# Optimization experiments

Hardware: AMD Instinct MI355X
Metric: run time of the kernel (lower is better)

## Reference

```python
import jax, jax.numpy as jnp
import numpy as np

EMBED_DIM = 1024
NUM_HEADS = 16
HEAD_DIM = EMBED_DIM // NUM_HEADS
BATCH = 2
SEQ = 2048


def setup_inputs() -> dict:
    key = jax.random.key(0)
    ks = jax.random.split(key, 9)
    s = EMBED_DIM ** -0.5
    inp = {"x": jax.random.normal(ks[0], (BATCH, SEQ, EMBED_DIM), dtype=jnp.float32)}
    names = ["Wq", "Wk", "Wv", "Wo"]
    for i, n in enumerate(names):
        inp[n] = jax.random.normal(ks[1 + i], (EMBED_DIM, EMBED_DIM), dtype=jnp.float32) * s
        inp["b" + n[1]] = jax.random.normal(ks[5 + i], (EMBED_DIM,), dtype=jnp.float32) * 0.02
    return inp


def reference(x, Wq, bq, Wk, bk, Wv, bv, Wo, bo):
    B, S, E = x.shape
    H, D = NUM_HEADS, HEAD_DIM
    scaling = D ** -0.5
    # projections (torch Linear: x @ W.T + b), reshape to (B, H, S, D)
    q = (x @ Wq.T + bq).reshape(B, S, H, D).transpose(0, 2, 1, 3)
    k = (x @ Wk.T + bk).reshape(B, S, H, D).transpose(0, 2, 1, 3)
    v = (x @ Wv.T + bv).reshape(B, S, H, D).transpose(0, 2, 1, 3)
    # full materialized score matrix, matching the original module
    scores = jnp.einsum("bhqd,bhkd->bhqk", q, k) * scaling
    causal = jnp.triu(jnp.ones((S, S), dtype=bool), k=1)  # True above diagonal
    scores = jnp.where(causal[None, None], -jnp.inf, scores)
    attn = jax.nn.softmax(scores, axis=-1)
    out = jnp.einsum("bhqk,bhkd->bhqd", attn, v)  # (B, H, S, D)
    out = out.transpose(0, 2, 1, 3).reshape(B, S, E)
    return out @ Wo.T + bo
```

## Files before the change

### kernel.cpp

```cpp
#include <hip/hip_runtime.h>
#include <stdint.h>

typedef __bf16 bf16;
typedef __bf16 bf16x8 __attribute__((ext_vector_type(8)));
typedef __bf16 bf16x4 __attribute__((ext_vector_type(4)));
typedef float  f32x4  __attribute__((ext_vector_type(4)));

#define E_DIM 1024
#define S_LEN 2048
#define BATCH 2
#define NH 16
#define DH 64

#define NEG_INF (-__builtin_inff())

__device__ __forceinline__ void load_lds16(const bf16* g, bf16* l) {
    __builtin_amdgcn_global_load_lds(
        (const __attribute__((address_space(1))) void*)g,
        (__attribute__((address_space(3))) void*)l, 16, 0, 0);
}

__global__ __launch_bounds__(256) void convert_kernel(
    const float* __restrict__ s0, const float* __restrict__ s1,
    const float* __restrict__ s2, const float* __restrict__ s3,
    const float* __restrict__ s4,
    bf16* __restrict__ d0, bf16* __restrict__ d1, bf16* __restrict__ d2,
    bf16* __restrict__ d3, bf16* __restrict__ d4,
    int n0, int n1)
{
    const float* src; bf16* dst; int n;
    switch (blockIdx.y) {
        case 0:  src = s0; dst = d0; n = n0; break;
        case 1:  src = s1; dst = d1; n = n1; break;
        case 2:  src = s2; dst = d2; n = n1; break;
        case 3:  src = s3; dst = d3; n = n1; break;
        default: src = s4; dst = d4; n = n1; break;
    }
    int i = (blockIdx.x * 256 + threadIdx.x) * 4;
    if (i >= n) return;
    float4 v = *(const float4*)(src + i);
    bf16x4 o;
    o[0] = (bf16)v.x; o[1] = (bf16)v.y; o[2] = (bf16)v.z; o[3] = (bf16)v.w;
    *(bf16x4*)(dst + i) = o;
}

__global__ __launch_bounds__(256) void gemm_kernel(
    const bf16* __restrict__ A,
    const bf16* __restrict__ W0, const bf16* __restrict__ W1, const bf16* __restrict__ W2,
    const float* __restrict__ bias0, const float* __restrict__ bias1, const float* __restrict__ bias2,
    bf16* __restrict__ outQ, bf16* __restrict__ outK, bf16* __restrict__ outVt,
    float* __restrict__ outF, int final_mode)
{
    __shared__ bf16 As[2][128 * 32];
    __shared__ bf16 Bs[2][128 * 32];

    int mode;
    const bf16* W; const float* bias;
    if (final_mode) { mode = 3; W = W0; bias = bias0; }
    else {
        mode = blockIdx.z;
        W    = (mode == 0) ? W0 : (mode == 1 ? W1 : W2);
        bias = (mode == 0) ? bias0 : (mode == 1 ? bias1 : bias2);
    }

    const int bm = blockIdx.y * 128, bn = blockIdx.x * 128;
    const int t = threadIdx.x;
    const int lane = t & 63, w = t >> 6;
    const int quad = lane >> 4, l16 = lane & 15;
    const int wm = (w & 1) * 64, wn = (w >> 1) * 64;

    const int r0 = w * 16;
    const int srow = r0 + (lane >> 2), scol = (lane & 3) * 8;
    const bf16* Ag0 = A + (size_t)(bm + srow) * E_DIM + scol;
    const bf16* Ag1 = Ag0 + (size_t)64 * E_DIM;
    const bf16* Wg0 = W + (size_t)(bn + srow) * E_DIM + scol;
    const bf16* Wg1 = Wg0 + (size_t)64 * E_DIM;

    f32x4 acc[4][4];
#pragma unroll
    for (int i = 0; i < 4; i++)
#pragma unroll
        for (int j = 0; j < 4; j++) acc[i][j] = f32x4{0.f, 0.f, 0.f, 0.f};

    load_lds16(Ag0, As[0] + r0 * 32);
    load_lds16(Ag1, As[0] + (64 + r0) * 32);
    load_lds16(Wg0, Bs[0] + r0 * 32);
    load_lds16(Wg1, Bs[0] + (64 + r0) * 32);

    int cur = 0;
    for (int kt = 0; kt < E_DIM; kt += 32) {
        __syncthreads();

        if (kt + 32 < E_DIM) {
            const int nxt = cur ^ 1;
            load_lds16(Ag0 + kt + 32, As[nxt] + r0 * 32);
            load_lds16(Ag1 + kt + 32, As[nxt] + (64 + r0) * 32);
            load_lds16(Wg0 + kt + 32, Bs[nxt] + r0 * 32);
            load_lds16(Wg1 + kt + 32, Bs[nxt] + (64 + r0) * 32);
        }

        bf16x8 af[4], bfr[4];
#pragma unroll
        for (int i = 0; i < 4; i++)
            af[i] = *(const bf16x8*)(As[cur] + (wm + i * 16 + l16) * 32 + quad * 8);
#pragma unroll
        for (int j = 0; j < 4; j++)
            bfr[j] = *(const bf16x8*)(Bs[cur] + (wn + j * 16 + l16) * 32 + quad * 8);
#pragma unroll
        for (int i = 0; i < 4; i++)
#pragma unroll
            for (int j = 0; j < 4; j++)
                acc[i][j] = __builtin_amdgcn_mfma_f32_16x16x32_bf16(af[i], bfr[j], acc[i][j], 0, 0, 0);

        cur ^= 1;
    }

#pragma unroll
    for (int j = 0; j < 4; j++) {
        const int n = bn + wn + j * 16 + l16;
        const float bv = bias[n];
#pragma unroll
        for (int i = 0; i < 4; i++) {
            const int m0 = bm + wm + i * 16 + quad * 4;
            if (mode == 3) {
#pragma unroll
                for (int r = 0; r < 4; r++)
                    outF[(size_t)(m0 + r) * E_DIM + n] = acc[i][j][r] + bv;
            } else if (mode == 2) {
                const int b_ = m0 >> 11, s0 = m0 & (S_LEN - 1);
                const int h = n >> 6, d = n & 63;
                bf16x4 pv;
#pragma unroll
                for (int r = 0; r < 4; r++) pv[r] = (bf16)(acc[i][j][r] + bv);
                *(bf16x4*)(outVt + ((size_t)((b_ * NH + h) * DH + d)) * S_LEN + s0) = pv;
            } else {
                bf16* o = (mode == 0) ? outQ : outK;
                const float sc = (mode == 0) ? 0.125f : 1.0f;
                const int h = n >> 6, d = n & 63;
#pragma unroll
                for (int r = 0; r < 4; r++) {
                    const int m = m0 + r;
                    const int b_ = m >> 11, s = m & (S_LEN - 1);
                    o[((size_t)(b_ * NH + h) * S_LEN + s) * DH + d] = (bf16)((acc[i][j][r] + bv) * sc);
                }
            }
        }
    }
}

__global__ __launch_bounds__(512, 2) void attn_kernel(
    const bf16* __restrict__ Qb, const bf16* __restrict__ Kb,
    const bf16* __restrict__ Vtb, bf16* __restrict__ Ob)
{
    __shared__ bf16 Ks[128 * 72];
    __shared__ bf16 Vs[64 * 136];
    __shared__ bf16 Ps[8][16 * 136];

    const int t = threadIdx.x, lane = t & 63, w = t >> 6;
    const int quad = lane >> 4, l16 = lane & 15;

    const int i = blockIdx.x;
    const int xcd = i & 7, rr = i >> 3;
    const int bh = (xcd << 2) | (rr & 3);
    const int pr = rr >> 2;
    const int qlo = pr, qhi = 15 - pr;

    const bf16* Qg = Qb + (size_t)bh * S_LEN * DH;
    const bf16* Kg = Kb + (size_t)bh * S_LEN * DH;
    const bf16* Vg = Vtb + (size_t)bh * DH * S_LEN;
    const int b_ = bh >> 4, h = bh & 15;
    bf16* Og = Ob + (size_t)b_ * S_LEN * E_DIM + h * DH;

    bf16* Pw = Ps[w];
    const int inrow0 = w * 16;

    bf16x8 aq[2][2];
#pragma unroll
    for (int qt = 0; qt < 2; qt++) {
        const int qrow0 = (qt ? qhi : qlo) * 128 + inrow0;
        const bf16* qp = Qg + (size_t)(qrow0 + l16) * DH + quad * 8;
        aq[qt][0] = *(const bf16x8*)(qp);
        aq[qt][1] = *(const bf16x8*)(qp + 32);
    }

    f32x4 o[2][4];
    float l_part[2][4];
#pragma unroll
    for (int qt = 0; qt < 2; qt++)
#pragma unroll
        for (int dt = 0; dt < 4; dt++) {
            o[qt][dt] = f32x4{0.f, 0.f, 0.f, 0.f};
            l_part[qt][dt] = 0.f;
        }

    const int T = qhi + 1;
    const int kr0 = t >> 3, kce = (t & 7) * 8;
    const int vr0 = t >> 4, vce = (t & 15) * 8;

    for (int kt = 0; kt < T; kt++) {
        const int kb = kt * 128;
        uint4 k0 = *(const uint4*)(Kg + (size_t)(kb + kr0) * DH + kce);
        uint4 k1 = *(const uint4*)(Kg + (size_t)(kb + kr0 + 64) * DH + kce);
        uint4 v0 = *(const uint4*)(Vg + (size_t)vr0 * S_LEN + kb + vce);
        uint4 v1 = *(const uint4*)(Vg + (size_t)(vr0 + 32) * S_LEN + kb + vce);
        __syncthreads();
        *(uint4*)(Ks + kr0 * 72 + kce) = k0;
        *(uint4*)(Ks + (kr0 + 64) * 72 + kce) = k1;
        *(uint4*)(Vs + vr0 * 136 + vce) = v0;
        *(uint4*)(Vs + (vr0 + 32) * 136 + vce) = v1;
        __syncthreads();

#pragma unroll
        for (int qt = 0; qt < 2; qt++) {
            if (qt == 0 && kt > qlo) continue;
            const bool diag = qt ? (kt == qhi) : (kt == qlo);
            const int irb = inrow0 + quad * 4;

#pragma unroll
            for (int jt = 0; jt < 8; jt++) {
                const bf16* kp = Ks + (jt * 16 + l16) * 72 + quad * 8;
                bf16x8 bk0 = *(const bf16x8*)(kp);
                bf16x8 bk1 = *(const bf16x8*)(kp + 32);
                f32x4 s = f32x4{0.f, 0.f, 0.f, 0.f};
                s = __builtin_amdgcn_mfma_f32_16x16x32_bf16(aq[qt][0], bk0, s, 0, 0, 0);
                s = __builtin_amdgcn_mfma_f32_16x16x32_bf16(aq[qt][1], bk1, s, 0, 0, 0);
                const int kcol = jt * 16 + l16;
#pragma unroll
                for (int r = 0; r < 4; r++) {
                    float sval = s[r];
                    if (diag && kcol > irb + r) sval = NEG_INF;
                    const float pe = __expf(sval);
                    l_part[qt][r] += pe;
                    Pw[(quad * 4 + r) * 136 + jt * 16 + l16] = (bf16)pe;
                }
            }

#pragma unroll
            for (int ks = 0; ks < 4; ks++) {
                bf16x8 ap = *(const bf16x8*)(Pw + l16 * 136 + ks * 32 + quad * 8);
#pragma unroll
                for (int dt = 0; dt < 4; dt++) {
                    bf16x8 bv = *(const bf16x8*)(Vs + (dt * 16 + l16) * 136 + ks * 32 + quad * 8);
                    o[qt][dt] = __builtin_amdgcn_mfma_f32_16x16x32_bf16(ap, bv, o[qt][dt], 0, 0, 0);
                }
            }
        }
    }

#pragma unroll
    for (int qt = 0; qt < 2; qt++) {
        const int qrow0 = (qt ? qhi : qlo) * 128 + inrow0;
#pragma unroll
        for (int r = 0; r < 4; r++) {
            float l = l_part[qt][r];
            l += __shfl_xor(l, 1);
            l += __shfl_xor(l, 2);
            l += __shfl_xor(l, 4);
            l += __shfl_xor(l, 8);
            l_part[qt][r] = 1.0f / l;
        }
#pragma unroll
        for (int r = 0; r < 4; r++) {
            const int srow = qrow0 + quad * 4 + r;
#pragma unroll
            for (int dt = 0; dt < 4; dt++)
                Og[(size_t)srow * E_DIM + dt * 16 + l16] =
                    (bf16)(o[qt][dt][r] * l_part[qt][r]);
        }
    }
}

extern "C" void kernel_launch(void* const* d_in, const int* in_sizes, int n_in,
                              void* d_out, int out_size, void* d_ws, size_t ws_size,
                              hipStream_t stream)
{
    const float* x  = (const float*)d_in[0];
    const float* Wq = (const float*)d_in[1];
    const float* bq = (const float*)d_in[2];
    const float* Wk = (const float*)d_in[3];
    const float* bk = (const float*)d_in[4];
    const float* Wv = (const float*)d_in[5];
    const float* bv = (const float*)d_in[6];
    const float* Wo = (const float*)d_in[7];
    const float* bo = (const float*)d_in[8];
    float* out = (float*)d_out;

    char* ws = (char*)d_ws;
    const size_t MB = 1ull << 20;
    bf16* xb  = (bf16*)(ws + 0);
    bf16* wqb = (bf16*)(ws + 8 * MB);
    bf16* wkb = (bf16*)(ws + 10 * MB);
    bf16* wvb = (bf16*)(ws + 12 * MB);
    bf16* wob = (bf16*)(ws + 14 * MB);
    bf16* Qb  = (bf16*)(ws + 16 * MB);
    bf16* Kb  = (bf16*)(ws + 24 * MB);
    bf16* Vtb = (bf16*)(ws + 32 * MB);
    bf16* Ab  = (bf16*)(ws + 40 * MB);

    convert_kernel<<<dim3(4096, 5), 256, 0, stream>>>(
        x, Wq, Wk, Wv, Wo, xb, wqb, wkb, wvb, wob, 4194304, 1048576);

    gemm_kernel<<<dim3(8, 32, 3), 256, 0, stream>>>(
        xb, wqb, wkb, wvb, bq, bk, bv, Qb, Kb, Vtb, nullptr, 0);

    attn_kernel<<<dim3(256), 512, 0, stream>>>(Qb, Kb, Vtb, Ab);

    gemm_kernel<<<dim3(8, 32, 1), 256, 0, stream>>>(
        Ab, wob, wob, wob, bo, bo, bo, nullptr, nullptr, nullptr, out, 1);
}
```

Measured before the change: 197.8 us.

## Fuse fp32-to-bf16 conversion into GEMM loads and pad LDS rows

Removes the separate convert kernel and has the GEMM read fp32 x and weights directly, converting to bf16 in registers before storing into LDS. Loads move from direct global-to-LDS to register-staged prefetch, and LDS rows are padded (32->40 in GEMM, 136->140 for P in attention) to cut bank conflicts. This removes one launch and the intermediate bf16 round trip, at the cost of re-reading fp32 x and weights from each tile (twice the bytes per reload) and more register pressure.

```diff
diff --git a/kernel.cpp b/kernel.cpp
--- a/kernel.cpp
+++ b/kernel.cpp
@@ -14,48 +14,25 @@
 
 #define NEG_INF (-__builtin_inff())
 
-__device__ __forceinline__ void load_lds16(const bf16* g, bf16* l) {
-    __builtin_amdgcn_global_load_lds(
-        (const __attribute__((address_space(1))) void*)g,
-        (__attribute__((address_space(3))) void*)l, 16, 0, 0);
+__device__ __forceinline__ bf16x8 cvt8(float4 u0, float4 u1) {
+    bf16x8 v;
+    v[0] = (bf16)u0.x; v[1] = (bf16)u0.y; v[2] = (bf16)u0.z; v[3] = (bf16)u0.w;
+    v[4] = (bf16)u1.x; v[5] = (bf16)u1.y; v[6] = (bf16)u1.z; v[7] = (bf16)u1.w;
+    return v;
 }
 
-__global__ __launch_bounds__(256) void convert_kernel(
-    const float* __restrict__ s0, const float* __restrict__ s1,
-    const float* __restrict__ s2, const float* __restrict__ s3,
-    const float* __restrict__ s4,
-    bf16* __restrict__ d0, bf16* __restrict__ d1, bf16* __restrict__ d2,
-    bf16* __restrict__ d3, bf16* __restrict__ d4,
-    int n0, int n1)
-{
-    const float* src; bf16* dst; int n;
-    switch (blockIdx.y) {
-        case 0:  src = s0; dst = d0; n = n0; break;
-        case 1:  src = s1; dst = d1; n = n1; break;
-        case 2:  src = s2; dst = d2; n = n1; break;
-        case 3:  src = s3; dst = d3; n = n1; break;
-        default: src = s4; dst = d4; n = n1; break;
-    }
-    int i = (blockIdx.x * 256 + threadIdx.x) * 4;
-    if (i >= n) return;
-    float4 v = *(const float4*)(src + i);
-    bf16x4 o;
-    o[0] = (bf16)v.x; o[1] = (bf16)v.y; o[2] = (bf16)v.z; o[3] = (bf16)v.w;
-    *(bf16x4*)(dst + i) = o;
-}
-
 __global__ __launch_bounds__(256) void gemm_kernel(
-    const bf16* __restrict__ A,
-    const bf16* __restrict__ W0, const bf16* __restrict__ W1, const bf16* __restrict__ W2,
+    const float* __restrict__ Af, const bf16* __restrict__ Abf,
+    const float* __restrict__ W0, const float* __restrict__ W1, const float* __restrict__ W2,
     const float* __restrict__ bias0, const float* __restrict__ bias1, const float* __restrict__ bias2,
     bf16* __restrict__ outQ, bf16* __restrict__ outK, bf16* __restrict__ outVt,
     float* __restrict__ outF, int final_mode)
 {
-    __shared__ bf16 As[2][128 * 32];
-    __shared__ bf16 Bs[2][128 * 32];
+    __shared__ bf16 As[2][128 * 40];
+    __shared__ bf16 Bs[2][128 * 40];
 
     int mode;
-    const bf16* W; const float* bias;
+    const float* W; const float* bias;
     if (final_mode) { mode = 3; W = W0; bias = bias0; }
     else {
         mode = blockIdx.z;
@@ -69,12 +46,15 @@
     const int quad = lane >> 4, l16 = lane & 15;
     const int wm = (w & 1) * 64, wn = (w >> 1) * 64;
 
-    const int r0 = w * 16;
-    const int srow = r0 + (lane >> 2), scol = (lane & 3) * 8;
-    const bf16* Ag0 = A + (size_t)(bm + srow) * E_DIM + scol;
-    const bf16* Ag1 = Ag0 + (size_t)64 * E_DIM;
-    const bf16* Wg0 = W + (size_t)(bn + srow) * E_DIM + scol;
-    const bf16* Wg1 = Wg0 + (size_t)64 * E_DIM;
+    const int r1 = t >> 2,          o1 = (t & 3) * 8;
+    const int r2 = (t + 256) >> 2,  o2 = (t & 3) * 8;
+
+    const float* Wg1 = W + (size_t)(bn + r1) * E_DIM + o1;
+    const float* Wg2 = W + (size_t)(bn + r2) * E_DIM + o2;
+    const float* Ag1f = Af  ? Af  + (size_t)(bm + r1) * E_DIM + o1 : nullptr;
+    const float* Ag2f = Af  ? Af  + (size_t)(bm + r2) * E_DIM + o2 : nullptr;
+    const bf16*  Ag1b = Abf ? Abf + (size_t)(bm + r1) * E_DIM + o1 : nullptr;
+    const bf16*  Ag2b = Abf ? Abf + (size_t)(bm + r2) * E_DIM + o2 : nullptr;
 
     f32x4 acc[4][4];
 #pragma unroll
@@ -82,30 +62,53 @@
 #pragma unroll
         for (int j = 0; j < 4; j++) acc[i][j] = f32x4{0.f, 0.f, 0.f, 0.f};
 
-    load_lds16(Ag0, As[0] + r0 * 32);
-    load_lds16(Ag1, As[0] + (64 + r0) * 32);
-    load_lds16(Wg0, Bs[0] + r0 * 32);
-    load_lds16(Wg1, Bs[0] + (64 + r0) * 32);
+    float4 wa0, wa1, wb0, wb1;
+    float4 aa0, aa1, ab0, ab1;
+    bf16x8 ba1, ba2;
+
+    wa0 = *(const float4*)(Wg1);  wa1 = *(const float4*)(Wg1 + 4);
+    wb0 = *(const float4*)(Wg2);  wb1 = *(const float4*)(Wg2 + 4);
+    if (final_mode) {
+        ba1 = *(const bf16x8*)(Ag1b);
+        ba2 = *(const bf16x8*)(Ag2b);
+    } else {
+        aa0 = *(const float4*)(Ag1f); aa1 = *(const float4*)(Ag1f + 4);
+        ab0 = *(const float4*)(Ag2f); ab1 = *(const float4*)(Ag2f + 4);
+    }
 
     int cur = 0;
     for (int kt = 0; kt < E_DIM; kt += 32) {
+        if (final_mode) {
+            *(bf16x8*)(As[cur] + r1 * 40 + o1) = ba1;
+            *(bf16x8*)(As[cur] + r2 * 40 + o2) = ba2;
+        } else {
+            *(bf16x8*)(As[cur] + r1 * 40 + o1) = cvt8(aa0, aa1);
+            *(bf16x8*)(As[cur] + r2 * 40 + o2) = cvt8(ab0, ab1);
+        }
+        *(bf16x8*)(Bs[cur] + r1 * 40 + o1) = cvt8(wa0, wa1);
+        *(bf16x8*)(Bs[cur] + r2 * 40 + o2) = cvt8(wb0, wb1);
         __syncthreads();
 
         if (kt + 32 < E_DIM) {
-            const int nxt = cur ^ 1;
-            load_lds16(Ag0 + kt + 32, As[nxt] + r0 * 32);
-            load_lds16(Ag1 + kt + 32, As[nxt] + (64 + r0) * 32);
-            load_lds16(Wg0 + kt + 32, Bs[nxt] + r0 * 32);
-            load_lds16(Wg1 + kt + 32, Bs[nxt] + (64 + r0) * 32);
+            const int nk = kt + 32;
+            wa0 = *(const float4*)(Wg1 + nk);  wa1 = *(const float4*)(Wg1 + nk + 4);
+            wb0 = *(const float4*)(Wg2 + nk);  wb1 = *(const float4*)(Wg2 + nk + 4);
+            if (final_mode) {
+                ba1 = *(const bf16x8*)(Ag1b + nk);
+                ba2 = *(const bf16x8*)(Ag2b + nk);
+            } else {
+                aa0 = *(const float4*)(Ag1f + nk); aa1 = *(const float4*)(Ag1f + nk + 4);
+                ab0 = *(const float4*)(Ag2f + nk); ab1 = *(const float4*)(Ag2f + nk + 4);
+            }
         }
 
         bf16x8 af[4], bfr[4];
 #pragma unroll
         for (int i = 0; i < 4; i++)
-            af[i] = *(const bf16x8*)(As[cur] + (wm + i * 16 + l16) * 32 + quad * 8);
+            af[i] = *(const bf16x8*)(As[cur] + (wm + i * 16 + l16) * 40 + quad * 8);
 #pragma unroll
         for (int j = 0; j < 4; j++)
-            bfr[j] = *(const bf16x8*)(Bs[cur] + (wn + j * 16 + l16) * 32 + quad * 8);
+            bfr[j] = *(const bf16x8*)(Bs[cur] + (wn + j * 16 + l16) * 40 + quad * 8);
 #pragma unroll
         for (int i = 0; i < 4; i++)
 #pragma unroll
@@ -154,7 +157,7 @@
 {
     __shared__ bf16 Ks[128 * 72];
     __shared__ bf16 Vs[64 * 136];
-    __shared__ bf16 Ps[8][16 * 136];
+    __shared__ bf16 Ps[8][16 * 140];
 
     const int t = threadIdx.x, lane = t & 63, w = t >> 6;
     const int quad = lane >> 4, l16 = lane & 15;
@@ -231,13 +234,13 @@
                     if (diag && kcol > irb + r) sval = NEG_INF;
                     const float pe = __expf(sval);
                     l_part[qt][r] += pe;
-                    Pw[(quad * 4 + r) * 136 + jt * 16 + l16] = (bf16)pe;
+                    Pw[(quad * 4 + r) * 140 + jt * 16 + l16] = (bf16)pe;
                 }
             }
 
 #pragma unroll
             for (int ks = 0; ks < 4; ks++) {
-                bf16x8 ap = *(const bf16x8*)(Pw + l16 * 136 + ks * 32 + quad * 8);
+                bf16x8 ap = *(const bf16x8*)(Pw + l16 * 140 + ks * 32 + quad * 8);
 #pragma unroll
                 for (int dt = 0; dt < 4; dt++) {
                     bf16x8 bv = *(const bf16x8*)(Vs + (dt * 16 + l16) * 136 + ks * 32 + quad * 8);
@@ -287,24 +290,16 @@
 
     char* ws = (char*)d_ws;
     const size_t MB = 1ull << 20;
-    bf16* xb  = (bf16*)(ws + 0);
-    bf16* wqb = (bf16*)(ws + 8 * MB);
-    bf16* wkb = (bf16*)(ws + 10 * MB);
-    bf16* wvb = (bf16*)(ws + 12 * MB);
-    bf16* wob = (bf16*)(ws + 14 * MB);
-    bf16* Qb  = (bf16*)(ws + 16 * MB);
-    bf16* Kb  = (bf16*)(ws + 24 * MB);
-    bf16* Vtb = (bf16*)(ws + 32 * MB);
-    bf16* Ab  = (bf16*)(ws + 40 * MB);
-
-    convert_kernel<<<dim3(4096, 5), 256, 0, stream>>>(
-        x, Wq, Wk, Wv, Wo, xb, wqb, wkb, wvb, wob, 4194304, 1048576);
+    bf16* Qb  = (bf16*)(ws + 0);
+    bf16* Kb  = (bf16*)(ws + 8 * MB);
+    bf16* Vtb = (bf16*)(ws + 16 * MB);
+    bf16* Ab  = (bf16*)(ws + 24 * MB);
 
     gemm_kernel<<<dim3(8, 32, 3), 256, 0, stream>>>(
-        xb, wqb, wkb, wvb, bq, bk, bv, Qb, Kb, Vtb, nullptr, 0);
+        x, nullptr, Wq, Wk, Wv, bq, bk, bv, Qb, Kb, Vtb, nullptr, 0);
 
     attn_kernel<<<dim3(256), 512, 0, stream>>>(Qb, Kb, Vtb, Ab);
 
     gemm_kernel<<<dim3(8, 32, 1), 256, 0, stream>>>(
-        Ab, wob, wob, wob, bo, bo, bo, nullptr, nullptr, nullptr, out, 1);
+        nullptr, Ab, Wo, Wo, Wo, bo, bo, bo, nullptr, nullptr, nullptr, out, 1);
 }
```

Result: slower. 232.2 us (+17.4%).
